# Performance work log

Hardware: AMD Instinct MI355X
Metric: run time of the kernel (lower is better)

## Reference

```python
import jax, jax.numpy as jnp
import numpy as np

N_DYADIC = 0   # init kwarg n: dyadic refinement order (0 = no refinement)


def _sig_kernel_gram(X, Y):
    """Signature-kernel Gram matrix via Goursat PDE solve (solver=0, linear kernel).

    X: (A, M, D), Y: (B, N, D). Returns K: (A, B) with K[a,b] = k_sig(x^a, y^b).
    PDE scheme: K[i+1,j+1] = K[i+1,j] + K[i,j+1] + K[i,j]*(inc[i,j] - 1),
    K[0,:] = K[:,0] = 1, inc[i,j] = <x_{i+1}-x_i, y_{j+1}-y_j>.
    The j-recursion is a prefix sum, so each row update is a vectorized cumsum;
    only the i-direction is sequential (lax.scan over M-1 rows).
    """
    dtype = X.dtype
    dX = X[:, 1:, :] - X[:, :-1, :]          # (A, M-1, D)
    dY = Y[:, 1:, :] - Y[:, :-1, :]          # (B, N-1, D)
    inc = jnp.einsum('amd,bnd->abmn', dX, dY)  # (A, B, M-1, N-1) increment grid
    if N_DYADIC > 0:
        f = 2 ** N_DYADIC
        inc = jnp.repeat(jnp.repeat(inc, f, axis=2), f, axis=3) / (f * f)
    A, B, M1, N1 = inc.shape
    ones_col = jnp.ones((A, B, 1), dtype)
    k0 = jnp.ones((A, B, N1 + 1), dtype)      # boundary row K[0, :] = 1

    def step(k_prev, inc_row):
        # k_new[j+1] = k_new[j] + (k_prev[j+1] - k_prev[j] + k_prev[j]*inc[j])
        delta = k_prev[..., 1:] - k_prev[..., :-1] + k_prev[..., :-1] * inc_row
        k_new = jnp.concatenate([ones_col, 1.0 + jnp.cumsum(delta, axis=-1)], axis=-1)
        return k_new, None

    k_last, _ = jax.lax.scan(step, k0, jnp.moveaxis(inc, 2, 0))
    return k_last[..., -1]                    # (A, B): K(s=T, t=T)


def setup_inputs() -> dict:
    key = jax.random.key(0)
    kx, ky = jax.random.split(key)
    # scale 0.1 keeps path increments moderate so the PDE solution stays well-conditioned
    X = jax.random.normal(kx, (64, 128, 64), dtype=jnp.float32) * 0.1
    Y = jax.random.normal(ky, (64, 128, 64), dtype=jnp.float32) * 0.1
    return {"X": X, "Y": Y}


def reference(X, Y):
    K_XX = _sig_kernel_gram(X, X)
    K_YY = _sig_kernel_gram(Y, Y)
    K_XY = _sig_kernel_gram(X, Y)
    dist = jnp.mean(K_XX) + jnp.mean(K_YY) - 2.0 * jnp.mean(K_XY)
    return jnp.mean((X[:, 0, :] - Y[:, 0, :]) ** 2) + dist
```

## Files before the change

kernel.cpp:

```cpp
#include <hip/hip_runtime.h>

#define AA   64
#define MM   128
#define DD   64
#define M1   127
#define CSTR 132
#define NXY  1024
#define NTRI 544
#define NBLK (NXY + 2*NTRI)
#define REG_I4 65536
#define PART_OFF (4u << 20)

typedef float f32x4 __attribute__((ext_vector_type(4)));
typedef short bf8_t __attribute__((ext_vector_type(8)));

template <int CTRL, int RM>
__device__ __forceinline__ float dpp0(float x) {
    return __int_as_float(
        __builtin_amdgcn_update_dpp(0, __float_as_int(x), CTRL, RM, 0xF, false));
}

__device__ __forceinline__ unsigned bf16_rne(float v) {
    unsigned u = __float_as_uint(v);
    return (u + 0x7FFFu + ((u >> 16) & 1u)) >> 16;
}
__device__ __forceinline__ float bf16_tof(unsigned h) {
    return __uint_as_float(h << 16);
}

__global__ __launch_bounds__(256) void prep_frags(const float* __restrict__ X,
                                                  const float* __restrict__ Y,
                                                  int4* __restrict__ frag) {
    const int tid = threadIdx.x, lane = tid & 63, w = tid >> 6;
    const int W    = blockIdx.x * 4 + w;
    const int inp  = W >> 9;
    const int p    = (W >> 3) & 63;
    const int tile = W & 7;
    const float* S = (inp ? Y : X) + p * (MM * DD);
    int i = tile * 16 + (lane & 15);
    if (i > 126) i = 126;
    const int d0 = (lane >> 4) << 3;

    int4* hi = frag + (inp * 2 + 0) * REG_I4;
    int4* lo = frag + (inp * 2 + 1) * REG_I4;
    const int base = p * 1024 + tile * 128 + lane;

    #pragma unroll
    for (int ks = 0; ks < 2; ++ks) {
        const float* r0 = S + i * DD + ks * 32 + d0;
        const float* r1 = r0 + DD;
        float4 a0 = *(const float4*)r0;
        float4 a1 = *(const float4*)(r0 + 4);
        float4 c0 = *(const float4*)r1;
        float4 c1 = *(const float4*)(r1 + 4);
        float v[8] = {c0.x - a0.x, c0.y - a0.y, c0.z - a0.z, c0.w - a0.w,
                      c1.x - a1.x, c1.y - a1.y, c1.z - a1.z, c1.w - a1.w};
        unsigned hs[8], ls[8];
        #pragma unroll
        for (int e = 0; e < 8; ++e) {
            hs[e] = bf16_rne(v[e]);
            ls[e] = bf16_rne(v[e] - bf16_tof(hs[e]));
        }
        int4 h, l;
        h.x = hs[0] | (hs[1] << 16); h.y = hs[2] | (hs[3] << 16);
        h.z = hs[4] | (hs[5] << 16); h.w = hs[6] | (hs[7] << 16);
        l.x = ls[0] | (ls[1] << 16); l.y = ls[2] | (ls[3] << 16);
        l.z = ls[4] | (ls[5] << 16); l.w = ls[6] | (ls[7] << 16);
        hi[base + ks * 64] = h;
        lo[base + ks * 64] = l;
    }
}

template <int ROWS>
__device__ __forceinline__ void load_sv(const float* incW, int c2l, float2* sv) {
    #pragma unroll
    for (int r = 0; r < ROWS; ++r)
        sv[r] = *(const float2*)(incW + r * CSTR + c2l);
}

template <int ROWS>
__device__ __forceinline__ void chain_sv(const float2* sv, int lane,
                                         float& Sv, float& e0p, float& e1p) {
    #pragma unroll
    for (int r = 0; r < ROWS; ++r) {
        float s0 = sv[r].x;
        float s1 = (lane < 63) ? sv[r].y : 0.0f;
        float Sp  = dpp0<0x138, 0xF>(Sv);
        float k0v = 1.0f + Sp;
        float k1v = 1.0f + Sv - e1p;
        float e0  = fmaf(k0v, s0, e0p);
        float e1  = fmaf(k1v, s1, e1p);
        float S   = e0 + e1;
        S += dpp0<0x111, 0xF>(S);
        S += dpp0<0x112, 0xF>(S);
        S += dpp0<0x114, 0xF>(S);
        S += dpp0<0x118, 0xF>(S);
        S += dpp0<0x142, 0xA>(S);
        S += dpp0<0x143, 0xC>(S);
        Sv = S; e0p = e0; e1p = e1;
    }
}

__global__ __launch_bounds__(256, 2)
void sig_pde(const int4* __restrict__ frag, float* __restrict__ partials) {
    const int tid = threadIdx.x, lane = tid & 63, w = tid >> 6;
    const int gid = blockIdx.x;

    int a, b, ain, bin;
    float wgt;
    if (gid < NXY) {
        b = gid >> 4; a = ((gid & 15) << 2) | w;
        ain = 0; bin = 1;
        wgt = -2.0f / 4096.0f;
    } else {
        int t = gid - NXY;
        int inp = 0;
        if (t >= NTRI) { t -= NTRI; inp = 1; }
        int q = (int)((__builtin_sqrtf((float)(2 * t + 1)) - 1.0f) * 0.5f);
        while (2 * (q + 1) * (q + 2) <= t) ++q;
        while (q > 0 && 2 * q * (q + 1) > t) --q;
        int r  = t - 2 * q * (q + 1);
        int i  = r / (q + 1);
        int ag = r - i * (q + 1);
        b = 4 * q + i; a = 4 * ag + w;
        ain = bin = inp;
        wgt = (a < b) ? (2.0f / 4096.0f) : ((a == b) ? (1.0f / 4096.0f) : 0.0f);
    }

    __shared__ int4  Bh[1024], Bl[1024];
    __shared__ float incS[4][16 * CSTR];
    __shared__ float red4[4];

    {
        const int4* Bhg = frag + (bin * 2 + 0) * REG_I4 + b * 1024;
        const int4* Blg = frag + (bin * 2 + 1) * REG_I4 + b * 1024;
        #pragma unroll
        for (int c = 0; c < 4; ++c) {
            int idx = c * 256 + tid;
            Bh[idx] = Bhg[idx];
            Bl[idx] = Blg[idx];
        }
    }
    __syncthreads();

    const int4* Ahg = frag + (ain * 2 + 0) * REG_I4 + a * 1024;
    const int4* Alg = frag + (ain * 2 + 1) * REG_I4 + a * 1024;

    int4 Ah[2][2], Al[2][2];
    f32x4 acc[2][8];
    float Sv = 0.0f, e0p = 0.0f, e1p = 0.0f;

    float* incW = &incS[w][0];
    const int c2l = lane << 1;
    const int r0w = (lane >> 4) << 2, c0w = lane & 15;

#define MFMA_PASS() do {                                                        \
    _Pragma("unroll")                                                           \
    for (int st_ = 0; st_ < 2; ++st_)                                           \
        _Pragma("unroll")                                                       \
        for (int t_ = 0; t_ < 8; ++t_) acc[st_][t_] = (f32x4){0.f,0.f,0.f,0.f}; \
    _Pragma("unroll")                                                           \
    for (int s_ = 0; s_ < 2; ++s_) {                                            \
        bf8_t ah0 = __builtin_bit_cast(bf8_t, Ah[0][s_]);                       \
        bf8_t al0 = __builtin_bit_cast(bf8_t, Al[0][s_]);                       \
        bf8_t ah1 = __builtin_bit_cast(bf8_t, Ah[1][s_]);                       \
        bf8_t al1 = __builtin_bit_cast(bf8_t, Al[1][s_]);                       \
        _Pragma("unroll")                                                       \
        for (int t_ = 0; t_ < 8; ++t_) {                                        \
            int fb = (t_ * 2 + s_) * 64 + lane;                                 \
            bf8_t bh = *(const bf8_t*)&Bh[fb];                                  \
            bf8_t bl = *(const bf8_t*)&Bl[fb];                                  \
            acc[0][t_] = __builtin_amdgcn_mfma_f32_16x16x32_bf16(ah0, bh, acc[0][t_], 0, 0, 0); \
            acc[1][t_] = __builtin_amdgcn_mfma_f32_16x16x32_bf16(ah1, bh, acc[1][t_], 0, 0, 0); \
            acc[0][t_] = __builtin_amdgcn_mfma_f32_16x16x32_bf16(ah0, bl, acc[0][t_], 0, 0, 0); \
            acc[1][t_] = __builtin_amdgcn_mfma_f32_16x16x32_bf16(ah1, bl, acc[1][t_], 0, 0, 0); \
            acc[0][t_] = __builtin_amdgcn_mfma_f32_16x16x32_bf16(al0, bh, acc[0][t_], 0, 0, 0); \
            acc[1][t_] = __builtin_amdgcn_mfma_f32_16x16x32_bf16(al1, bh, acc[1][t_], 0, 0, 0); \
        }                                                                       \
    }                                                                           \
} while (0)

#define STORE_STRIP(st) do {                                   \
    _Pragma("unroll")                                          \
    for (int t_ = 0; t_ < 8; ++t_) {                           \
        float* pb = incW + r0w * CSTR + (t_ << 4) + c0w;       \
        pb[0]        = acc[st][t_][0];                         \
        pb[CSTR]     = acc[st][t_][1];                         \
        pb[2 * CSTR] = acc[st][t_][2];                         \
        pb[3 * CSTR] = acc[st][t_][3];                         \
    }                                                          \
} while (0)

#define LOAD_A(poff) do {                                      \
    int off = (poff) + lane;                                   \
    Ah[0][0] = Ahg[off];       Ah[0][1] = Ahg[off + 64];       \
    Al[0][0] = Alg[off];       Al[0][1] = Alg[off + 64];       \
    Ah[1][0] = Ahg[off + 128]; Ah[1][1] = Ahg[off + 192];      \
    Al[1][0] = Alg[off + 128]; Al[1][1] = Alg[off + 192];      \
} while (0)

    LOAD_A(0);
    MFMA_PASS();

    for (int pass = 0; pass < 4; ++pass) {
        STORE_STRIP(0);
        if (pass < 3) LOAD_A((pass + 1) * 256);
        {
            float2 sv[16];
            load_sv<16>(incW, c2l, sv);
            chain_sv<16>(sv, lane, Sv, e0p, e1p);
        }
        STORE_STRIP(1);
        if (pass < 3) {
            float2 sv[16];
            load_sv<16>(incW, c2l, sv);
            MFMA_PASS();
            chain_sv<16>(sv, lane, Sv, e0p, e1p);
        } else {
            float2 sv[15];
            load_sv<15>(incW, c2l, sv);
            chain_sv<15>(sv, lane, Sv, e0p, e1p);
        }
    }

    if (lane == 63) red4[w] = wgt * (1.0f + Sv - e1p);
    __syncthreads();
    if (tid == 0)
        partials[gid] = red4[0] + red4[1] + red4[2] + red4[3];

#undef MFMA_PASS
#undef STORE_STRIP
#undef LOAD_A
}

__global__ void final_sum(const float* __restrict__ X, const float* __restrict__ Y,
                          const float* __restrict__ partials, float* __restrict__ out) {
    __shared__ float red[4];
    int tid = threadIdx.x;
    float acc = 0.f;
    for (int e = tid; e < NBLK; e += 256) acc += partials[e];
    for (int e = tid; e < AA * DD; e += 256) {
        int aa = e >> 6, d = e & 63;
        float df = X[aa * (MM * DD) + d] - Y[aa * (MM * DD) + d];
        acc = fmaf(df * df, 1.0f / 4096.0f, acc);
    }
    #pragma unroll
    for (int off = 32; off > 0; off >>= 1) acc += __shfl_down(acc, off);
    if ((tid & 63) == 0) red[tid >> 6] = acc;
    __syncthreads();
    if (tid == 0) out[0] = red[0] + red[1] + red[2] + red[3];
}

extern "C" void kernel_launch(void* const* d_in, const int* in_sizes, int n_in,
                              void* d_out, int out_size, void* d_ws, size_t ws_size,
                              hipStream_t stream) {
    const float* X = (const float*)d_in[0];
    const float* Y = (const float*)d_in[1];
    float* out = (float*)d_out;
    int4*  frag = (int4*)d_ws;
    float* partials = (float*)((char*)d_ws + PART_OFF);

    hipLaunchKernelGGL(prep_frags, dim3(256), dim3(256), 0, stream, X, Y, frag);
    hipLaunchKernelGGL(sig_pde, dim3(NBLK), dim3(256), 0, stream, frag, partials);
    hipLaunchKernelGGL(final_sum, dim3(1), dim3(256), 0, stream, X, Y, partials, out);
}
```

Before: 147.6 us.

## Halve per-wave LDS increment strip and raise occupancy to three blocks per CU

The per-wave increment staging buffer is cut from 16 to 8 rows. Each 16-row MFMA strip is now stored and read back in two 8-row halves, with explicit LDS waitcnt fences between halves. The smaller LDS footprint and launch bound of 3 are meant to fit more blocks per CU and hide latency of the sequential chain. The tighter register budget risks spills, and the extra fences serialize LDS traffic.

```diff
diff --git a/kernel.cpp b/kernel.cpp
--- a/kernel.cpp
+++ b/kernel.cpp
@@ -26,6 +26,11 @@
 }
 __device__ __forceinline__ float bf16_tof(unsigned h) {
     return __uint_as_float(h << 16);
+}
+
+__device__ __forceinline__ void lds_fence() {
+    asm volatile("s_waitcnt lgkmcnt(0)" ::: "memory");
+    __builtin_amdgcn_sched_barrier(0);
 }
 
 __global__ __launch_bounds__(256) void prep_frags(const float* __restrict__ X,
@@ -101,7 +106,7 @@
     }
 }
 
-__global__ __launch_bounds__(256, 2)
+__global__ __launch_bounds__(256, 3)
 void sig_pde(const int4* __restrict__ frag, float* __restrict__ partials) {
     const int tid = threadIdx.x, lane = tid & 63, w = tid >> 6;
     const int gid = blockIdx.x;
@@ -128,7 +133,7 @@
     }
 
     __shared__ int4  Bh[1024], Bl[1024];
-    __shared__ float incS[4][16 * CSTR];
+    __shared__ float incS[4][8 * CSTR];
     __shared__ float red4[4];
 
     {
@@ -180,14 +185,17 @@
     }                                                                           \
 } while (0)
 
-#define STORE_STRIP(st) do {                                   \
-    _Pragma("unroll")                                          \
-    for (int t_ = 0; t_ < 8; ++t_) {                           \
-        float* pb = incW + r0w * CSTR + (t_ << 4) + c0w;       \
-        pb[0]        = acc[st][t_][0];                         \
-        pb[CSTR]     = acc[st][t_][1];                         \
-        pb[2 * CSTR] = acc[st][t_][2];                         \
-        pb[3 * CSTR] = acc[st][t_][3];                         \
+#define STORE_H(st, half) do {                                 \
+    if ((r0w & 8) == ((half) << 3)) {                          \
+        float* pb = incW + (r0w & 7) * CSTR + c0w;             \
+        _Pragma("unroll")                                      \
+        for (int t_ = 0; t_ < 8; ++t_) {                       \
+            float* q = pb + (t_ << 4);                         \
+            q[0]        = acc[st][t_][0];                      \
+            q[CSTR]     = acc[st][t_][1];                      \
+            q[2 * CSTR] = acc[st][t_][2];                      \
+            q[3 * CSTR] = acc[st][t_][3];                      \
+        }                                                      \
     }                                                          \
 } while (0)
 
@@ -203,23 +211,35 @@
     MFMA_PASS();
 
     for (int pass = 0; pass < 4; ++pass) {
-        STORE_STRIP(0);
         if (pass < 3) LOAD_A((pass + 1) * 256);
+
         {
-            float2 sv[16];
-            load_sv<16>(incW, c2l, sv);
-            chain_sv<16>(sv, lane, Sv, e0p, e1p);
-        }
-        STORE_STRIP(1);
+            float2 svA[8], svB[8];
+            lds_fence(); STORE_H(0, 0);
+            load_sv<8>(incW, c2l, svA);
+            lds_fence(); STORE_H(0, 1);
+            load_sv<8>(incW, c2l, svB);
+            chain_sv<8>(svA, lane, Sv, e0p, e1p);
+            chain_sv<8>(svB, lane, Sv, e0p, e1p);
+        }
+
         if (pass < 3) {
-            float2 sv[16];
-            load_sv<16>(incW, c2l, sv);
+            float2 svA[8], svB[8];
+            lds_fence(); STORE_H(1, 0);
+            load_sv<8>(incW, c2l, svA);
+            lds_fence(); STORE_H(1, 1);
+            load_sv<8>(incW, c2l, svB);
             MFMA_PASS();
-            chain_sv<16>(sv, lane, Sv, e0p, e1p);
+            chain_sv<8>(svA, lane, Sv, e0p, e1p);
+            chain_sv<8>(svB, lane, Sv, e0p, e1p);
         } else {
-            float2 sv[15];
-            load_sv<15>(incW, c2l, sv);
-            chain_sv<15>(sv, lane, Sv, e0p, e1p);
+            float2 svA[8], svB[7];
+            lds_fence(); STORE_H(1, 0);
+            load_sv<8>(incW, c2l, svA);
+            lds_fence(); STORE_H(1, 1);
+            load_sv<7>(incW, c2l, svB);
+            chain_sv<8>(svA, lane, Sv, e0p, e1p);
+            chain_sv<7>(svB, lane, Sv, e0p, e1p);
         }
     }
 
@@ -229,7 +249,7 @@
         partials[gid] = red4[0] + red4[1] + red4[2] + red4[3];
 
 #undef MFMA_PASS
-#undef STORE_STRIP
+#undef STORE_H
 #undef LOAD_A
 }
 
```

Measured after the change: 238.9 us. 61.8% more time.
